# Kernel tuning notes

Hardware: AMD Instinct MI355X
Metric: run time of the kernel (lower is better)

The kernel has to match this reference:

```python
import jax, jax.numpy as jnp
import numpy as np

B, T, C = 32, 512, 32
D, H, DFF, NL = 512, 8, 2048, 3
P, STRIDE, PAD = 16, 8, 8
N = (T - P) // STRIDE + 2  # 64 patches
E = D // H


def _sinusoidal_pe(n, d):
    pos = np.arange(n, dtype=np.float32)[:, None]
    div = np.exp(np.arange(0, d, 2, dtype=np.float32) * -(np.log(10000.0) / d))
    pe = np.zeros((n, d), np.float32)
    pe[:, 0::2] = np.sin(pos * div)
    pe[:, 1::2] = np.cos(pos * div)
    return jnp.asarray(pe)


def setup_inputs() -> dict:
    key = jax.random.key(0)
    ks = jax.random.split(key, 16)
    s = 0.02
    inp = {
        'x_enc': jax.random.normal(ks[0], (B, T, C), jnp.float32),
        'W_val': jax.random.normal(ks[1], (P, D), jnp.float32) * s,
        'Wq': jax.random.normal(ks[2], (NL, D, D), jnp.float32) * s,
        'bq': jnp.zeros((NL, D), jnp.float32),
        'Wk': jax.random.normal(ks[3], (NL, D, D), jnp.float32) * s,
        'bk': jnp.zeros((NL, D), jnp.float32),
        'Wv': jax.random.normal(ks[4], (NL, D, D), jnp.float32) * s,
        'bv': jnp.zeros((NL, D), jnp.float32),
        'Wo': jax.random.normal(ks[5], (NL, D, D), jnp.float32) * s,
        'bo': jnp.zeros((NL, D), jnp.float32),
        'Wc1': jax.random.normal(ks[6], (NL, D, DFF), jnp.float32) * s,
        'bc1': jnp.zeros((NL, DFF), jnp.float32),
        'Wc2': jax.random.normal(ks[7], (NL, DFF, D), jnp.float32) * s,
        'bc2': jnp.zeros((NL, D), jnp.float32),
        'ln1_g': jnp.ones((NL, D), jnp.float32),
        'ln1_b': jnp.zeros((NL, D), jnp.float32),
        'ln2_g': jnp.ones((NL, D), jnp.float32),
        'ln2_b': jnp.zeros((NL, D), jnp.float32),
        'bn_g': jnp.ones((D,), jnp.float32),
        'bn_b': jnp.zeros((D,), jnp.float32),
        'W_head': jax.random.normal(ks[8], (D * N, T), jnp.float32) * s,
        'b_head': jnp.zeros((T,), jnp.float32),
    }
    return inp


def _ln(x, g, b, eps=1e-5):
    m = x.mean(-1, keepdims=True)
    v = ((x - m) ** 2).mean(-1, keepdims=True)
    return (x - m) / jnp.sqrt(v + eps) * g + b


def reference(x_enc, W_val, Wq, bq, Wk, bk, Wv, bv, Wo, bo, Wc1, bc1, Wc2, bc2,
              ln1_g, ln1_b, ln2_g, ln2_b, bn_g, bn_b, W_head, b_head):
    pe = _sinusoidal_pe(N, D)
    # instance normalization over time (means detached, as in torch .detach())
    means = jax.lax.stop_gradient(x_enc.mean(axis=1, keepdims=True))
    x = x_enc - means
    stdev = jnp.sqrt(x.var(axis=1, keepdims=True) + 1e-5)  # [B,1,C]
    x = x / stdev
    x = x.transpose(0, 2, 1)  # [B, C, T]
    # replication pad right by PAD, then unfold into patches [B,C,N,P]
    x = jnp.concatenate([x, jnp.broadcast_to(x[..., -1:], x.shape[:-1] + (PAD,))], axis=-1)
    idx = jnp.arange(N)[:, None] * STRIDE + jnp.arange(P)[None, :]
    xp = x[..., idx]
    tok = xp.reshape(B * C, N, P) @ W_val + pe  # [B*C, N, D]

    scale = 1.0 / np.sqrt(E).astype(np.float32)
    for i in range(NL):
        q = (tok @ Wq[i] + bq[i]).reshape(-1, N, H, E)
        k = (tok @ Wk[i] + bk[i]).reshape(-1, N, H, E)
        v = (tok @ Wv[i] + bv[i]).reshape(-1, N, H, E)
        scores = jnp.einsum('blhe,bshe->bhls', q, k)
        A = jax.nn.softmax(scale * scores, axis=-1)
        V = jnp.einsum('bhls,bshd->blhd', A, v).reshape(-1, N, D)
        tok = tok + (V @ Wo[i] + bo[i])
        y = _ln(tok, ln1_g[i], ln1_b[i])
        y = jax.nn.gelu(y @ Wc1[i] + bc1[i], approximate=False) @ Wc2[i] + bc2[i]
        tok = _ln(tok + y, ln2_g[i], ln2_b[i])

    # BatchNorm1d over d_model channels (batch statistics, biased variance)
    m = tok.mean(axis=(0, 1))
    var = tok.var(axis=(0, 1))
    tok = (tok - m) / jnp.sqrt(var + 1e-5) * bn_g + bn_b

    enc = tok.reshape(B, C, N, D).transpose(0, 1, 3, 2).reshape(B, C, D * N)
    dec = enc @ W_head + b_head          # [B, C, T]
    dec = dec.transpose(0, 2, 1)          # [B, T, C]
    dec = dec * stdev[:, 0, :][:, None, :] + means[:, 0, :][:, None, :]
    return dec
```

## Files before the change

kernel.cpp:

```cpp
#include <hip/hip_runtime.h>
#include <math.h>

namespace {
constexpr int kB = 32, kT = 512, kC = 32, kD = 512, kDFF = 2048, kNL = 3;
constexpr int kP = 16, kStride = 8, kN = 64;
constexpr int kR = kB * kC;
constexpr int kM = kR * kN;
constexpr size_t kWbElems = (size_t)1536 * 512 + 512 * 512 + 2048 * 512 + 512 * 2048;
}

typedef unsigned short u16;
typedef __attribute__((ext_vector_type(8))) short short8;
typedef __attribute__((ext_vector_type(4))) float f32x4;

__device__ __forceinline__ float b2f(u16 u) {
    return __uint_as_float(((unsigned int)u) << 16);
}
__device__ __forceinline__ u16 f2b(float f) {
    unsigned int x = __float_as_uint(f);
    return (u16)((x + 0x7fffu + ((x >> 16) & 1u)) >> 16);
}

__device__ __forceinline__ void async_copy16(const void* g, void* l) {
    __builtin_amdgcn_global_load_lds(
        (const __attribute__((address_space(1))) unsigned int*)g,
        (__attribute__((address_space(3))) unsigned int*)l, 16, 0, 0);
}

__global__ void fill_kernel(float* __restrict__ p, float val, int n)
{
    int i = blockIdx.x * blockDim.x + threadIdx.x;
    if (i < n) p[i] = val;
}

__global__ __launch_bounds__(256) void instnorm_stats_kernel(
    const float* __restrict__ x, float* __restrict__ means, float* __restrict__ stdev)
{
    int b = blockIdx.x;
    int c = threadIdx.x & 31;
    int g = threadIdx.x >> 5;
    float s = 0.f, sq = 0.f;
    for (int t = g; t < kT; t += 8) {
        float v = x[(size_t)(b * kT + t) * kC + c];
        s += v; sq += v * v;
    }
    __shared__ float ss[8][32], ssq[8][32];
    ss[g][c] = s; ssq[g][c] = sq;
    __syncthreads();
    if (g == 0) {
        float S = 0.f, SQ = 0.f;
        for (int i = 0; i < 8; i++) { S += ss[i][c]; SQ += ssq[i][c]; }
        float m = S / kT;
        float var = SQ / kT - m * m;
        means[b * kC + c] = m;
        stdev[b * kC + c] = sqrtf(var + 1e-5f);
    }
}

__global__ __launch_bounds__(256) void patch_embed_kernel(
    const float* __restrict__ x, const float* __restrict__ Wval,
    const float* __restrict__ means, const float* __restrict__ stdev,
    u16* __restrict__ tok)
{
    int m = blockIdx.x;
    int r = m >> 6, n = m & 63;
    int b = r >> 5, c = r & 31;
    __shared__ float patch[kP];
    if (threadIdx.x < kP) {
        int t = n * kStride + threadIdx.x;
        if (t > kT - 1) t = kT - 1;
        patch[threadIdx.x] = (x[(size_t)(b * kT + t) * kC + c] - means[r]) / stdev[r];
    }
    __syncthreads();
    for (int d = threadIdx.x; d < kD; d += 256) {
        float acc = 0.f;
        #pragma unroll
        for (int p = 0; p < kP; p++) acc += patch[p] * Wval[p * kD + d];
        int j = d >> 1;
        float freq = expf(-(float)(2 * j) * (9.210340371976184f / (float)kD));
        float ang = (float)n * freq;
        float pe = (d & 1) ? cosf(ang) : sinf(ang);
        tok[(size_t)m * kD + d] = f2b(acc + pe);
    }
}

__global__ __launch_bounds__(256) void transpose_cvt_kernel(
    const float* __restrict__ in, u16* __restrict__ outp,
    int ldi, int ldo, int zin, int zout)
{
    __shared__ float tile[64][65];
    const float* ib = in + (size_t)blockIdx.z * zin;
    u16* ob = outp + (size_t)blockIdx.z * zout;
    int k0 = blockIdx.x * 64, n0 = blockIdx.y * 64;
    int tn = threadIdx.x & 63, tk0 = threadIdx.x >> 6;
    #pragma unroll
    for (int kk = tk0; kk < 64; kk += 4)
        tile[kk][tn] = ib[(size_t)(k0 + kk) * ldi + n0 + tn];
    __syncthreads();
    int wk = threadIdx.x & 63, wn0 = threadIdx.x >> 6;
    #pragma unroll
    for (int nn = wn0; nn < 64; nn += 4)
        ob[(size_t)(n0 + nn) * ldo + k0 + wk] = f2b(tile[wk][nn]);
}

template<int EPI>
__global__ __launch_bounds__(512, 2) void gemm8(
    const u16* __restrict__ A, const u16* __restrict__ B,
    const float* __restrict__ bias, const float* __restrict__ auxb1,
    const float* __restrict__ auxb2,
    u16* __restrict__ C0, u16* __restrict__ C1, u16* __restrict__ C2,
    float* __restrict__ fout, const float* __restrict__ stdev,
    int K, int lda, int ldb, int ldc)
{
    __shared__ u16 sm[65536];
    u16* const bufA0 = sm;
    u16* const bufB0 = sm + 16384;
    u16* const bufA1 = sm + 32768;
    u16* const bufB1 = sm + 49152;

    const int tid  = threadIdx.x;
    const int lane = tid & 63;
    const int wave = tid >> 6;
    const int wm   = wave >> 2;
    const int wn   = wave & 3;

    const int nwg  = gridDim.x * gridDim.y;
    const int orig = blockIdx.y * gridDim.x + blockIdx.x;
    const int qq = nwg >> 3, rr = nwg & 7;
    const int xcd = orig & 7, loc = orig >> 3;
    const int wg  = (xcd < rr) ? (xcd * (qq + 1) + loc)
                               : (rr * (qq + 1) + (xcd - rr) * qq + loc);
    const int row0 = (wg / gridDim.x) * 256;
    const int col0 = (wg % gridDim.x) * 256;
    const size_t zoff = (size_t)blockIdx.z * K;

    const int srow = (wave << 3) + (lane >> 3);
    const int scol = ((lane & 7) ^ (lane >> 3)) << 3;
    const u16* const Ag = A + (size_t)(row0 + srow) * lda + zoff + scol;
    const u16* const Bg = B + (size_t)(col0 + srow) * ldb + zoff + scol;
    const int lw = wave << 3;

#define STAGE_A(BUF, R0, T) do { \
        const u16* g_ = Ag + (size_t)(R0) * lda + (T) * 64; \
        u16* l_ = bufA##BUF + (((R0) + lw) << 6); \
        async_copy16(g_, l_); \
        async_copy16(g_ + (size_t)64 * lda, l_ + (64 << 6)); \
    } while (0)
#define STAGE_B(BUF, R0, T) do { \
        const u16* g_ = Bg + (size_t)(R0) * ldb + (T) * 64; \
        u16* l_ = bufB##BUF + (((R0) + lw) << 6); \
        async_copy16(g_, l_); \
        async_copy16(g_ + (size_t)64 * ldb, l_ + (64 << 6)); \
    } while (0)

    const int fr = lane & 15;
    const int pc = (lane >> 4) ^ (lane & 7);
    const int a0 = ((wm << 7) + fr) * 64 + pc * 8;
    const int a1 = ((wm << 7) + fr) * 64 + (pc ^ 4) * 8;
    const int b0 = ((wn << 6) + fr) * 64 + pc * 8;
    const int b1 = ((wn << 6) + fr) * 64 + (pc ^ 4) * 8;

    short8 af[8][2], bfr[4][2];
    f32x4 acc[8][4];
    #pragma unroll
    for (int i = 0; i < 8; i++)
        #pragma unroll
        for (int j = 0; j < 4; j++)
            acc[i][j] = (f32x4){0.f, 0.f, 0.f, 0.f};

#define RD_A(BUF, MH) do { \
        _Pragma("unroll") \
        for (int mi_ = 0; mi_ < 4; mi_++) { \
            af[(MH)*4 + mi_][0] = *(const short8*)&bufA##BUF[a0 + (((MH)*4 + mi_) << 10)]; \
            af[(MH)*4 + mi_][1] = *(const short8*)&bufA##BUF[a1 + (((MH)*4 + mi_) << 10)]; \
        } \
    } while (0)
#define RD_B(BUF, NH) do { \
        _Pragma("unroll") \
        for (int ni_ = 0; ni_ < 2; ni_++) { \
            bfr[(NH)*2 + ni_][0] = *(const short8*)&bufB##BUF[b0 + (((NH)*2 + ni_) << 10)]; \
            bfr[(NH)*2 + ni_][1] = *(const short8*)&bufB##BUF[b1 + (((NH)*2 + ni_) << 10)]; \
        } \
    } while (0)
#define MFMA_Q(MH, NH) do { \
        __builtin_amdgcn_s_setprio(1); \
        _Pragma("unroll") \
        for (int mi_ = 0; mi_ < 4; mi_++) \
            _Pragma("unroll") \
            for (int ni_ = 0; ni_ < 2; ni_++) { \
                acc[(MH)*4 + mi_][(NH)*2 + ni_] = __builtin_amdgcn_mfma_f32_16x16x32_bf16( \
                    af[(MH)*4 + mi_][0], bfr[(NH)*2 + ni_][0], \
                    acc[(MH)*4 + mi_][(NH)*2 + ni_], 0, 0, 0); \
                acc[(MH)*4 + mi_][(NH)*2 + ni_] = __builtin_amdgcn_mfma_f32_16x16x32_bf16( \
                    af[(MH)*4 + mi_][1], bfr[(NH)*2 + ni_][1], \
                    acc[(MH)*4 + mi_][(NH)*2 + ni_], 0, 0, 0); \
            } \
        __builtin_amdgcn_s_setprio(0); \
    } while (0)
#define BAR() __builtin_amdgcn_s_barrier()
#define VM_FENCE(N) asm volatile("s_waitcnt vmcnt(" #N ")" ::: "memory")

    STAGE_A(0, 0, 0);  STAGE_A(0, 128, 0);
    STAGE_B(0, 0, 0);  STAGE_B(0, 128, 0);
    STAGE_A(1, 0, 1);  STAGE_A(1, 128, 1);
    VM_FENCE(4);
    BAR();

    const int nIter = K >> 7;
    for (int it = 0; it < nIter; it++) {
        const int t1 = 2 * it + 1, t2 = 2 * it + 2, t3 = 2 * it + 3;
        const bool full = (it < nIter - 1);
        RD_A(0, 0); RD_B(0, 0);
        STAGE_B(1, 0, t1);
        BAR(); MFMA_Q(0, 0); BAR();
        RD_A(0, 1); RD_B(0, 1);
        STAGE_B(1, 128, t1);
        BAR(); MFMA_Q(1, 0); BAR();
        if (full) STAGE_A(0, 0, t2);
        BAR(); MFMA_Q(0, 1); BAR();
        if (full) { STAGE_A(0, 128, t2); VM_FENCE(4); }
        else      { VM_FENCE(0); }
        BAR(); MFMA_Q(1, 1); BAR();
        RD_A(1, 0); RD_B(1, 0);
        if (full) STAGE_B(0, 0, t2);
        BAR(); MFMA_Q(0, 0); BAR();
        RD_A(1, 1); RD_B(1, 1);
        if (full) STAGE_B(0, 128, t2);
        BAR(); MFMA_Q(1, 0); BAR();
        if (full) STAGE_A(1, 0, t3);
        BAR(); MFMA_Q(0, 1); BAR();
        if (full) { STAGE_A(1, 128, t3); VM_FENCE(4); }
        BAR(); MFMA_Q(1, 1); BAR();
    }

    const int er = (lane >> 4) << 2;
    const int ec = lane & 15;
    u16* dsel = C0;
    const float* bsel = bias;
    if (EPI == 0) {
        int sub = col0 >> 9;
        dsel = (sub == 0) ? C0 : ((sub == 1) ? C1 : C2);
        bsel = (sub == 0) ? bias : ((sub == 1) ? auxb1 : auxb2);
    }
    #pragma unroll
    for (int mi = 0; mi < 8; mi++) {
        #pragma unroll
        for (int ni = 0; ni < 4; ni++) {
            #pragma unroll
            for (int i = 0; i < 4; i++) {
                int r  = row0 + (wm << 7) + (mi << 4) + er + i;
                int cc = col0 + (wn << 6) + (ni << 4) + ec;
                float v = acc[mi][ni][i];
                if (EPI == 0) {
                    int cl = cc & 511;
                    dsel[(size_t)r * 512 + cl] = f2b(v + bsel[cl]);
                } else if (EPI == 1) {
                    size_t o = (size_t)r * ldc + cc;
                    float bb2 = bias ? bias[cc] : 0.f;
                    C0[o] = f2b(b2f(C0[o]) + v + bb2);
                } else if (EPI == 2) {
                    size_t o = (size_t)r * ldc + cc;
                    float z = v + bias[cc];
                    C0[o] = f2b(0.5f * z * (1.f + erff(z * 0.7071067811865475f)));
                } else {
                    float vv = v * stdev[r];
                    atomicAdd(&fout[(((size_t)(r >> 5) * kT + cc) << 5) + (r & 31)], vv);
                }
            }
        }
    }
#undef STAGE_A
#undef STAGE_B
#undef RD_A
#undef RD_B
#undef MFMA_Q
#undef BAR
#undef VM_FENCE
}

__global__ __launch_bounds__(256) void attn_mfma_kernel(
    u16* __restrict__ qbuf, const u16* __restrict__ kbuf,
    const u16* __restrict__ vbuf)
{
    __shared__ u16 P[4][64 * 64];
    const int tid = threadIdx.x;
    const int wave = tid >> 6, lane = tid & 63;
    const int quad = lane >> 4, l15 = lane & 15;
    const size_t base = (size_t)blockIdx.x * 64 * kD;
    u16* Pw = P[wave];

    for (int hh = 0; hh < 2; hh++) {
        const int h = wave * 2 + hh;
        const u16* qh = qbuf + base + h * 64;
        const u16* kh = kbuf + base + h * 64;
        const u16* vh = vbuf + base + h * 64;

        short8 af[4][2], bf[4][2];
        #pragma unroll
        for (int mi = 0; mi < 4; mi++)
            #pragma unroll
            for (int kt = 0; kt < 2; kt++)
                af[mi][kt] = *(const short8*)(qh + (size_t)(mi * 16 + l15) * kD
                                              + kt * 32 + quad * 8);
        #pragma unroll
        for (int ni = 0; ni < 4; ni++)
            #pragma unroll
            for (int kt = 0; kt < 2; kt++)
                bf[ni][kt] = *(const short8*)(kh + (size_t)(ni * 16 + l15) * kD
                                              + kt * 32 + quad * 8);
        f32x4 S[4][4];
        #pragma unroll
        for (int mi = 0; mi < 4; mi++)
            #pragma unroll
            for (int ni = 0; ni < 4; ni++)
                S[mi][ni] = (f32x4){0.f, 0.f, 0.f, 0.f};
        #pragma unroll
        for (int mi = 0; mi < 4; mi++)
            #pragma unroll
            for (int ni = 0; ni < 4; ni++) {
                S[mi][ni] = __builtin_amdgcn_mfma_f32_16x16x32_bf16(
                    af[mi][0], bf[ni][0], S[mi][ni], 0, 0, 0);
                S[mi][ni] = __builtin_amdgcn_mfma_f32_16x16x32_bf16(
                    af[mi][1], bf[ni][1], S[mi][ni], 0, 0, 0);
            }

        #pragma unroll
        for (int mi = 0; mi < 4; mi++) {
            #pragma unroll
            for (int i = 0; i < 4; i++) {
                float mx = -1e30f;
                #pragma unroll
                for (int ni = 0; ni < 4; ni++) {
                    float v = S[mi][ni][i] * 0.125f;
                    S[mi][ni][i] = v;
                    mx = fmaxf(mx, v);
                }
                #pragma unroll
                for (int off = 1; off < 16; off <<= 1)
                    mx = fmaxf(mx, __shfl_xor(mx, off));
                float sum = 0.f;
                #pragma unroll
                for (int ni = 0; ni < 4; ni++) {
                    float e = expf(S[mi][ni][i] - mx);
                    S[mi][ni][i] = e;
                    sum += e;
                }
                #pragma unroll
                for (int off = 1; off < 16; off <<= 1)
                    sum += __shfl_xor(sum, off);
                float inv = 1.f / sum;
                #pragma unroll
                for (int ni = 0; ni < 4; ni++)
                    Pw[(mi * 16 + quad * 4 + i) * 64 + ni * 16 + l15] =
                        f2b(S[mi][ni][i] * inv);
            }
        }
        __syncthreads();

        short8 bv[4][2];
        #pragma unroll
        for (int ni = 0; ni < 4; ni++)
            #pragma unroll
            for (int kt = 0; kt < 2; kt++)
                #pragma unroll
                for (int j = 0; j < 8; j++)
                    bv[ni][kt][j] = (short)vh[(size_t)(kt * 32 + quad * 8 + j) * kD
                                              + ni * 16 + l15];
        short8 pa[4][2];
        #pragma unroll
        for (int mi = 0; mi < 4; mi++)
            #pragma unroll
            for (int kt = 0; kt < 2; kt++)
                pa[mi][kt] = *(const short8*)&Pw[(mi * 16 + l15) * 64
                                                 + kt * 32 + quad * 8];
        f32x4 O[4][4];
        #pragma unroll
        for (int mi = 0; mi < 4; mi++)
            #pragma unroll
            for (int ni = 0; ni < 4; ni++)
                O[mi][ni] = (f32x4){0.f, 0.f, 0.f, 0.f};
        #pragma unroll
        for (int mi = 0; mi < 4; mi++)
            #pragma unroll
            for (int ni = 0; ni < 4; ni++) {
                O[mi][ni] = __builtin_amdgcn_mfma_f32_16x16x32_bf16(
                    pa[mi][0], bv[ni][0], O[mi][ni], 0, 0, 0);
                O[mi][ni] = __builtin_amdgcn_mfma_f32_16x16x32_bf16(
                    pa[mi][1], bv[ni][1], O[mi][ni], 0, 0, 0);
            }
        u16* qo = qbuf + base + h * 64;
        #pragma unroll
        for (int mi = 0; mi < 4; mi++)
            #pragma unroll
            for (int ni = 0; ni < 4; ni++)
                #pragma unroll
                for (int i = 0; i < 4; i++)
                    qo[(size_t)(mi * 16 + quad * 4 + i) * kD + ni * 16 + l15] =
                        f2b(O[mi][ni][i]);
        __syncthreads();
    }
}

__global__ __launch_bounds__(256) void ln_kernel(
    const u16* __restrict__ x, const float* __restrict__ g,
    const float* __restrict__ bb, u16* __restrict__ y)
{
    size_t row = (size_t)blockIdx.x * 4 + (threadIdx.x >> 6);
    int lane = threadIdx.x & 63;
    float v[8];
    float s = 0.f;
    #pragma unroll
    for (int i = 0; i < 8; i++) {
        v[i] = b2f(x[row * kD + lane + i * 64]);
        s += v[i];
    }
    #pragma unroll
    for (int off = 32; off; off >>= 1) s += __shfl_xor(s, off);
    float mean = s * (1.f / kD);
    float sq = 0.f;
    #pragma unroll
    for (int i = 0; i < 8; i++) { float d = v[i] - mean; sq += d * d; }
    #pragma unroll
    for (int off = 32; off; off >>= 1) sq += __shfl_xor(sq, off);
    float inv = 1.f / sqrtf(sq * (1.f / kD) + 1e-5f);
    #pragma unroll
    for (int i = 0; i < 8; i++) {
        int d = lane + i * 64;
        y[row * kD + d] = f2b((v[i] - mean) * inv * g[d] + bb[d]);
    }
}

__global__ void zero_kernel(float* __restrict__ p, int n)
{
    int i = blockIdx.x * blockDim.x + threadIdx.x;
    if (i < n) p[i] = 0.f;
}

__global__ __launch_bounds__(512) void bn_stats_kernel(
    const u16* __restrict__ tok, float* __restrict__ sums, float* __restrict__ sumsq)
{
    int d = threadIdx.x;
    float s = 0.f, sq = 0.f;
    int row0 = blockIdx.x * 256;
    for (int row = row0; row < row0 + 256; row++) {
        float v = b2f(tok[(size_t)row * kD + d]);
        s += v; sq += v * v;
    }
    atomicAdd(&sums[d], s);
    atomicAdd(&sumsq[d], sq);
}

__global__ __launch_bounds__(512) void bn_final_kernel(
    const float* __restrict__ sums, const float* __restrict__ sumsq,
    const float* __restrict__ g, const float* __restrict__ bb,
    float* __restrict__ scale, float* __restrict__ shift)
{
    int d = threadIdx.x;
    float mean = sums[d] / (float)kM;
    float var = sumsq[d] / (float)kM - mean * mean;
    float sc = g[d] / sqrtf(var + 1e-5f);
    scale[d] = sc;
    shift[d] = bb[d] - mean * sc;
}

__global__ __launch_bounds__(256) void bn_apply_kernel(
    u16* __restrict__ tok, const float* __restrict__ scale,
    const float* __restrict__ shift)
{
    size_t i = (size_t)blockIdx.x * 256 + threadIdx.x;
    int d = (int)(i & 511);
    tok[i] = f2b(b2f(tok[i]) * scale[d] + shift[d]);
}

__global__ __launch_bounds__(256) void head_init_kernel(
    float* __restrict__ out, const float* __restrict__ b_head,
    const float* __restrict__ stdev, const float* __restrict__ means)
{
    int i = blockIdx.x * 256 + threadIdx.x;
    int c = i & 31, t = (i >> 5) & 511, b = i >> 14;
    int r = b * 32 + c;
    out[i] = b_head[t] * stdev[r] + means[r];
}

extern "C" void kernel_launch(void* const* d_in, const int* in_sizes, int n_in,
                              void* d_out, int out_size, void* d_ws, size_t ws_size,
                              hipStream_t stream)
{
    const float* x_enc  = (const float*)d_in[0];
    const float* W_val  = (const float*)d_in[1];
    const float* Wq     = (const float*)d_in[2];
    const float* bq     = (const float*)d_in[3];
    const float* Wk     = (const float*)d_in[4];
    const float* bk     = (const float*)d_in[5];
    const float* Wv     = (const float*)d_in[6];
    const float* bv     = (const float*)d_in[7];
    const float* Wo     = (const float*)d_in[8];
    const float* bo     = (const float*)d_in[9];
    const float* Wc1    = (const float*)d_in[10];
    const float* bc1    = (const float*)d_in[11];
    const float* Wc2    = (const float*)d_in[12];
    const float* bc2    = (const float*)d_in[13];
    const float* ln1_g  = (const float*)d_in[14];
    const float* ln1_b  = (const float*)d_in[15];
    const float* ln2_g  = (const float*)d_in[16];
    const float* ln2_b  = (const float*)d_in[17];
    const float* bn_g   = (const float*)d_in[18];
    const float* bn_b   = (const float*)d_in[19];
    const float* W_head = (const float*)d_in[20];
    const float* b_head = (const float*)d_in[21];
    float* out = (float*)d_out;

    const size_t tailBytes = (2 * kR + 4 * kD) * sizeof(float);
    const size_t headWb = (size_t)512 * 32768;
    int CH = 0; size_t unit = 0, region = 0;
    const int cands[4] = {1024, 512, 256, 128};
    for (int ci = 0; ci < 4; ci++) {
        size_t u = (size_t)cands[ci] * 64 * kD;
        size_t reg = 3 * u + kWbElems;
        if (reg < headWb) reg = headWb;
        size_t need = ((size_t)kM * kD + reg) * 2 + tailBytes;
        if (need <= ws_size) { CH = cands[ci]; unit = u; region = reg; break; }
    }
    if (CH == 0) {
        hipLaunchKernelGGL(fill_kernel, dim3((out_size + 255) / 256), dim3(256), 0,
                           stream, out, 1.0e6f, out_size);
        return;
    }
    const int nch = kR / CH;
    const int chRows = CH * 64;

    u16* tokb = (u16*)d_ws;
    u16* s0  = tokb + (size_t)kM * kD;
    u16* s1  = s0 + unit;
    u16* s2  = s1 + unit;
    u16* wbL = s2 + unit;
    u16* wbH = s0;
    u16* wQKV = wbL;
    u16* wO   = wQKV + (size_t)1536 * 512;
    u16* wC1  = wO + (size_t)512 * 512;
    u16* wC2  = wC1 + (size_t)2048 * 512;
    float* tail = (float*)(s0 + region);
    float* means    = tail;
    float* stdevp   = means + kR;
    float* bn_sums  = stdevp + kR;
    float* bn_sumsq = bn_sums + kD;
    float* bn_scale = bn_sumsq + kD;
    float* bn_shift = bn_scale + kD;

    hipLaunchKernelGGL(instnorm_stats_kernel, dim3(kB), dim3(256), 0, stream,
                       x_enc, means, stdevp);
    hipLaunchKernelGGL(patch_embed_kernel, dim3(kM), dim3(256), 0, stream,
                       x_enc, W_val, means, stdevp, tokb);

    const dim3 blk(256);
    const dim3 blk512(512);
    const dim3 tr8(8, 8, 1);
    const int mt256 = chRows / 256;

    for (int i = 0; i < kNL; i++) {
        const float* Wq_i = Wq + (size_t)i * kD * kD;
        const float* Wk_i = Wk + (size_t)i * kD * kD;
        const float* Wv_i = Wv + (size_t)i * kD * kD;
        const float* Wo_i = Wo + (size_t)i * kD * kD;
        const float* Wc1_i = Wc1 + (size_t)i * kD * kDFF;
        const float* Wc2_i = Wc2 + (size_t)i * kDFF * kD;
        const float* bq_i = bq + i * kD, *bk_i = bk + i * kD, *bv_i = bv + i * kD;

        hipLaunchKernelGGL(transpose_cvt_kernel, tr8, blk, 0, stream,
                           Wq_i, wQKV, kD, kD, 0, 0);
        hipLaunchKernelGGL(transpose_cvt_kernel, tr8, blk, 0, stream,
                           Wk_i, wQKV + (size_t)512 * 512, kD, kD, 0, 0);
        hipLaunchKernelGGL(transpose_cvt_kernel, tr8, blk, 0, stream,
                           Wv_i, wQKV + (size_t)1024 * 512, kD, kD, 0, 0);
        hipLaunchKernelGGL(transpose_cvt_kernel, tr8, blk, 0, stream,
                           Wo_i, wO, kD, kD, 0, 0);
        hipLaunchKernelGGL(transpose_cvt_kernel, dim3(8, 32, 1), blk, 0, stream,
                           Wc1_i, wC1, kDFF, kD, 0, 0);
        hipLaunchKernelGGL(transpose_cvt_kernel, dim3(32, 8, 1), blk, 0, stream,
                           Wc2_i, wC2, kD, kDFF, 0, 0);

        for (int ch = 0; ch < nch; ch++) {
            u16* tokc = tokb + (size_t)ch * chRows * kD;
            hipLaunchKernelGGL((gemm8<0>), dim3(6, mt256, 1), blk512, 0, stream,
                               tokc, wQKV, bq_i, bk_i, bv_i, s0, s1, s2,
                               nullptr, nullptr, kD, kD, kD, kD);
            hipLaunchKernelGGL(attn_mfma_kernel, dim3(CH), blk, 0, stream,
                               s0, s1, s2);
            hipLaunchKernelGGL((gemm8<1>), dim3(2, mt256, 1), blk512, 0, stream,
                               s0, wO, bo + i * kD, nullptr, nullptr,
                               tokc, nullptr, nullptr, nullptr, nullptr,
                               kD, kD, kD, kD);
            hipLaunchKernelGGL(ln_kernel, dim3(chRows / 4), blk, 0, stream,
                               tokc, ln1_g + i * kD, ln1_b + i * kD, s0);
            for (int half = 0; half < 2; half++) {
                const u16* wc1h = wC1 + (size_t)half * 1024 * 512;
                const u16* wc2h = wC2 + (size_t)half * 1024;
                const float* bc1h = bc1 + (size_t)i * kDFF + half * 1024;
                hipLaunchKernelGGL((gemm8<2>), dim3(4, mt256, 1), blk512, 0, stream,
                                   s0, wc1h, bc1h, nullptr, nullptr,
                                   s1, nullptr, nullptr, nullptr, nullptr,
                                   kD, kD, kD, 1024);
                hipLaunchKernelGGL((gemm8<1>), dim3(2, mt256, 1), blk512, 0, stream,
                                   s1, wc2h, (half == 0) ? (bc2 + i * kD) : nullptr,
                                   nullptr, nullptr, tokc, nullptr, nullptr,
                                   nullptr, nullptr, 1024, 1024, kDFF, kD);
            }
            hipLaunchKernelGGL(ln_kernel, dim3(chRows / 4), blk, 0, stream,
                               tokc, ln2_g + i * kD, ln2_b + i * kD, tokc);
        }
    }

    hipLaunchKernelGGL(zero_kernel, dim3(1), dim3(1024), 0, stream, bn_sums, 2 * kD);
    hipLaunchKernelGGL(bn_stats_kernel, dim3(kM / 256), dim3(512), 0, stream,
                       tokb, bn_sums, bn_sumsq);
    hipLaunchKernelGGL(bn_final_kernel, dim3(1), dim3(512), 0, stream,
                       bn_sums, bn_sumsq, bn_g, bn_b, bn_scale, bn_shift);
    hipLaunchKernelGGL(bn_apply_kernel, dim3((int)((size_t)kM * kD / 256)), blk, 0,
                       stream, tokb, bn_scale, bn_shift);

    hipLaunchKernelGGL(transpose_cvt_kernel, dim3(8, 8, 64), blk, 0, stream,
                       W_head, wbH, 64 * 512, 32768, 512, 512);
    hipLaunchKernelGGL(head_init_kernel, dim3(out_size / 256), blk, 0, stream,
                       out, b_head, stdevp, means);
    hipLaunchKernelGGL((gemm8<3>), dim3(2, 4, 32), blk512, 0, stream,
                       tokb, wbH, nullptr, nullptr, nullptr,
                       nullptr, nullptr, nullptr, out, stdevp,
                       1024, 32768, 32768, kT);
}
```

Baseline: 3.743 ms.

## Restructure GEMM mainloop into triple-buffered K=32 tiles with sched barriers

Replaces the double-buffered 64-wide K staging in the bf16 MFMA GEMM with a three-stage ring of 32-wide K tiles (six 16 KB LDS buffers), prefetching two tiles ahead. It uses a new XOR swizzle for the narrower rows, one MFMA per fragment pair, and sched_barrier fences to pin instruction order. The aim is to hide global-to-LDS latency better with a deeper pipeline. The cost is more barriers per K unit, since each 32-wide tile takes four barriers, and shorter MFMA bursts between synchronisation points.

```diff
diff --git a/kernel.cpp b/kernel.cpp
--- a/kernel.cpp
+++ b/kernel.cpp
@@ -21,7 +21,7 @@
     return (u16)((x + 0x7fffu + ((x >> 16) & 1u)) >> 16);
 }
 
-__device__ __forceinline__ void async_copy16(const void* g, void* l) {
+__device__ __forceinline__ void async_copy16(const u16* g, u16* l) {
     __builtin_amdgcn_global_load_lds(
         (const __attribute__((address_space(1))) unsigned int*)g,
         (__attribute__((address_space(3))) unsigned int*)l, 16, 0, 0);
@@ -112,11 +112,12 @@
     float* __restrict__ fout, const float* __restrict__ stdev,
     int K, int lda, int ldb, int ldc)
 {
-    __shared__ u16 sm[65536];
-    u16* const bufA0 = sm;
-    u16* const bufB0 = sm + 16384;
-    u16* const bufA1 = sm + 32768;
-    u16* const bufB1 = sm + 49152;
+    __shared__ alignas(16) u16 A0s[8192];
+    __shared__ alignas(16) u16 B0s[8192];
+    __shared__ alignas(16) u16 A1s[8192];
+    __shared__ alignas(16) u16 B1s[8192];
+    __shared__ alignas(16) u16 A2s[8192];
+    __shared__ alignas(16) u16 B2s[8192];
 
     const int tid  = threadIdx.x;
     const int lane = tid & 63;
@@ -134,33 +135,24 @@
     const int col0 = (wg % gridDim.x) * 256;
     const size_t zoff = (size_t)blockIdx.z * K;
 
-    const int srow = (wave << 3) + (lane >> 3);
-    const int scol = ((lane & 7) ^ (lane >> 3)) << 3;
+    const int srow = tid >> 2;
+    const int scol = (((tid & 3) ^ (srow & 3)) << 3);
     const u16* const Ag = A + (size_t)(row0 + srow) * lda + zoff + scol;
     const u16* const Bg = B + (size_t)(col0 + srow) * ldb + zoff + scol;
-    const int lw = wave << 3;
-
-#define STAGE_A(BUF, R0, T) do { \
-        const u16* g_ = Ag + (size_t)(R0) * lda + (T) * 64; \
-        u16* l_ = bufA##BUF + (((R0) + lw) << 6); \
-        async_copy16(g_, l_); \
-        async_copy16(g_ + (size_t)64 * lda, l_ + (64 << 6)); \
+    const int woff = wave << 9;
+
+#define STG(Lp, Gp, ld, T) do { \
+        const u16* g0_ = (Gp) + (size_t)(T) * 32; \
+        async_copy16(g0_, (Lp) + woff); \
+        async_copy16(g0_ + (size_t)128 * (ld), (Lp) + 4096 + woff); \
     } while (0)
-#define STAGE_B(BUF, R0, T) do { \
-        const u16* g_ = Bg + (size_t)(R0) * ldb + (T) * 64; \
-        u16* l_ = bufB##BUF + (((R0) + lw) << 6); \
-        async_copy16(g_, l_); \
-        async_copy16(g_ + (size_t)64 * ldb, l_ + (64 << 6)); \
-    } while (0)
 
     const int fr = lane & 15;
-    const int pc = (lane >> 4) ^ (lane & 7);
-    const int a0 = ((wm << 7) + fr) * 64 + pc * 8;
-    const int a1 = ((wm << 7) + fr) * 64 + (pc ^ 4) * 8;
-    const int b0 = ((wn << 6) + fr) * 64 + pc * 8;
-    const int b1 = ((wn << 6) + fr) * 64 + (pc ^ 4) * 8;
-
-    short8 af[8][2], bfr[4][2];
+    const int pc = (lane >> 4) ^ (lane & 3);
+    const int aoff = ((((wm << 7) + fr) << 5)) + (pc << 3);
+    const int boff = ((((wn << 6) + fr) << 5)) + (pc << 3);
+
+    short8 af[4], bfr[4];
     f32x4 acc[8][4];
     #pragma unroll
     for (int i = 0; i < 8; i++)
@@ -168,70 +160,55 @@
         for (int j = 0; j < 4; j++)
             acc[i][j] = (f32x4){0.f, 0.f, 0.f, 0.f};
 
-#define RD_A(BUF, MH) do { \
+#define RDA(Lp, MH) do { \
         _Pragma("unroll") \
-        for (int mi_ = 0; mi_ < 4; mi_++) { \
-            af[(MH)*4 + mi_][0] = *(const short8*)&bufA##BUF[a0 + (((MH)*4 + mi_) << 10)]; \
-            af[(MH)*4 + mi_][1] = *(const short8*)&bufA##BUF[a1 + (((MH)*4 + mi_) << 10)]; \
-        } \
+        for (int mi_ = 0; mi_ < 4; mi_++) \
+            af[mi_] = *(const short8*)&(Lp)[aoff + ((MH) << 11) + (mi_ << 9)]; \
     } while (0)
-#define RD_B(BUF, NH) do { \
+#define RDB(Lp) do { \
         _Pragma("unroll") \
-        for (int ni_ = 0; ni_ < 2; ni_++) { \
-            bfr[(NH)*2 + ni_][0] = *(const short8*)&bufB##BUF[b0 + (((NH)*2 + ni_) << 10)]; \
-            bfr[(NH)*2 + ni_][1] = *(const short8*)&bufB##BUF[b1 + (((NH)*2 + ni_) << 10)]; \
-        } \
+        for (int ni_ = 0; ni_ < 4; ni_++) \
+            bfr[ni_] = *(const short8*)&(Lp)[boff + (ni_ << 9)]; \
     } while (0)
-#define MFMA_Q(MH, NH) do { \
+#define MFMAH(MH) do { \
         __builtin_amdgcn_s_setprio(1); \
         _Pragma("unroll") \
         for (int mi_ = 0; mi_ < 4; mi_++) \
             _Pragma("unroll") \
-            for (int ni_ = 0; ni_ < 2; ni_++) { \
-                acc[(MH)*4 + mi_][(NH)*2 + ni_] = __builtin_amdgcn_mfma_f32_16x16x32_bf16( \
-                    af[(MH)*4 + mi_][0], bfr[(NH)*2 + ni_][0], \
-                    acc[(MH)*4 + mi_][(NH)*2 + ni_], 0, 0, 0); \
-                acc[(MH)*4 + mi_][(NH)*2 + ni_] = __builtin_amdgcn_mfma_f32_16x16x32_bf16( \
-                    af[(MH)*4 + mi_][1], bfr[(NH)*2 + ni_][1], \
-                    acc[(MH)*4 + mi_][(NH)*2 + ni_], 0, 0, 0); \
-            } \
+            for (int ni_ = 0; ni_ < 4; ni_++) \
+                acc[(MH) * 4 + mi_][ni_] = __builtin_amdgcn_mfma_f32_16x16x32_bf16( \
+                    af[mi_], bfr[ni_], acc[(MH) * 4 + mi_][ni_], 0, 0, 0); \
         __builtin_amdgcn_s_setprio(0); \
     } while (0)
 #define BAR() __builtin_amdgcn_s_barrier()
-#define VM_FENCE(N) asm volatile("s_waitcnt vmcnt(" #N ")" ::: "memory")
-
-    STAGE_A(0, 0, 0);  STAGE_A(0, 128, 0);
-    STAGE_B(0, 0, 0);  STAGE_B(0, 128, 0);
-    STAGE_A(1, 0, 1);  STAGE_A(1, 128, 1);
-    VM_FENCE(4);
-    BAR();
-
-    const int nIter = K >> 7;
-    for (int it = 0; it < nIter; it++) {
-        const int t1 = 2 * it + 1, t2 = 2 * it + 2, t3 = 2 * it + 3;
-        const bool full = (it < nIter - 1);
-        RD_A(0, 0); RD_B(0, 0);
-        STAGE_B(1, 0, t1);
-        BAR(); MFMA_Q(0, 0); BAR();
-        RD_A(0, 1); RD_B(0, 1);
-        STAGE_B(1, 128, t1);
-        BAR(); MFMA_Q(1, 0); BAR();
-        if (full) STAGE_A(0, 0, t2);
-        BAR(); MFMA_Q(0, 1); BAR();
-        if (full) { STAGE_A(0, 128, t2); VM_FENCE(4); }
-        else      { VM_FENCE(0); }
-        BAR(); MFMA_Q(1, 1); BAR();
-        RD_A(1, 0); RD_B(1, 0);
-        if (full) STAGE_B(0, 0, t2);
-        BAR(); MFMA_Q(0, 0); BAR();
-        RD_A(1, 1); RD_B(1, 1);
-        if (full) STAGE_B(0, 128, t2);
-        BAR(); MFMA_Q(1, 0); BAR();
-        if (full) STAGE_A(1, 0, t3);
-        BAR(); MFMA_Q(0, 1); BAR();
-        if (full) { STAGE_A(1, 128, t3); VM_FENCE(4); }
-        BAR(); MFMA_Q(1, 1); BAR();
-    }
+#define SB0() __builtin_amdgcn_sched_barrier(0)
+#define VMF(N) asm volatile("s_waitcnt vmcnt(" #N ")")
+
+#define WINDOW(RA, RB, SA, SB, T) do { \
+        const bool st_ = ((T) + 2 < nT); \
+        RDA(RA, 0); RDB(RB); \
+        if (st_) { STG(SA, Ag, lda, (T) + 2); STG(SB, Bg, ldb, (T) + 2); } \
+        BAR(); SB0(); MFMAH(0); BAR(); SB0(); \
+        RDA(RA, 1); \
+        BAR(); SB0(); MFMAH(1); \
+        if (st_) { VMF(4); } else if ((T) + 1 < nT) { VMF(0); } \
+        BAR(); SB0(); \
+    } while (0)
+
+    const int nT = K >> 5;
+    STG(A0s, Ag, lda, 0); STG(B0s, Bg, ldb, 0);
+    STG(A1s, Ag, lda, 1); STG(B1s, Bg, ldb, 1);
+    VMF(4);
+    BAR(); SB0();
+
+    int t = 0;
+    for (; t + 3 <= nT; t += 3) {
+        WINDOW(A0s, B0s, A2s, B2s, t);
+        WINDOW(A1s, B1s, A0s, B0s, t + 1);
+        WINDOW(A2s, B2s, A1s, B1s, t + 2);
+    }
+    if (t < nT) { WINDOW(A0s, B0s, A2s, B2s, t); t++; }
+    if (t < nT) { WINDOW(A1s, B1s, A0s, B0s, t); t++; }
 
     const int er = (lane >> 4) << 2;
     const int ec = lane & 15;
@@ -269,13 +246,14 @@
             }
         }
     }
-#undef STAGE_A
-#undef STAGE_B
-#undef RD_A
-#undef RD_B
-#undef MFMA_Q
+#undef STG
+#undef RDA
+#undef RDB
+#undef MFMAH
 #undef BAR
-#undef VM_FENCE
+#undef SB0
+#undef VMF
+#undef WINDOW
 }
 
 __global__ __launch_bounds__(256) void attn_mfma_kernel(
```

New measurement: 3.477 ms. 1.08x faster.
